# Performance work log

Measured on AMD Instinct MI355X. Metric: run time of the kernel, lower is better.

## Reference

```python
import jax, jax.numpy as jnp
import numpy as np

B = 8            # scenes per batch
N_PER = 100_000  # voxels per scene
C_IN = 32
C_OUT = 64
GRID = 128       # voxel grid extent per axis
K = 8            # 2x2x2 kernel offsets
EPS = 1e-5


def _kernel_maps():
    """Build stride-2 sparse-conv kernel maps (MinkowskiEngine semantics).

    Each input voxel at coord c maps to output voxel floor(c/2) with kernel
    offset c - 2*floor(c/2) in {0,1}^3.
    """
    rng = np.random.default_rng(0)
    coords = rng.integers(0, GRID, size=(B * N_PER, 3)).astype(np.int64)
    batch = np.repeat(np.arange(B, dtype=np.int64), N_PER)
    out_c = coords // 2
    off = coords - 2 * out_c                      # {0,1}^3
    k_idx = off[:, 0] * 4 + off[:, 1] * 2 + off[:, 2]
    half = GRID // 2
    key = ((batch * half + out_c[:, 0]) * half + out_c[:, 1]) * half + out_c[:, 2]
    _, out_idx = np.unique(key, return_inverse=True)
    num_out = int(out_idx.max()) + 1
    return k_idx.astype(np.int32), out_idx.astype(np.int32), num_out


def setup_inputs() -> dict:
    k_idx_np, out_idx_np, num_out = _kernel_maps()
    key = jax.random.key(0)
    k1, k2, k3 = jax.random.split(key, 3)
    x = jax.random.normal(k1, (B * N_PER, C_IN), dtype=jnp.float32)
    W = jax.random.normal(k2, (K, C_IN, C_OUT), dtype=jnp.float32) * 0.05
    bias = jax.random.normal(k3, (C_OUT,), dtype=jnp.float32) * 0.01
    gamma = jnp.ones((C_OUT,), dtype=jnp.float32)
    beta = jnp.zeros((C_OUT,), dtype=jnp.float32)
    return {
        "x": x, "W": W, "bias": bias, "gamma": gamma, "beta": beta,
        "k_idx": jnp.asarray(k_idx_np), "out_idx": jnp.asarray(out_idx_np),
        "num_out": num_out,
    }


def reference(x, W, bias, gamma, beta, k_idx, out_idx, num_out):
    # Sparse conv (gather-GEMM-scatter). Each input voxel uses exactly one of
    # the 8 kernel weights (stride==kernel_size==2), so y[i] = x[i] @ W[k_idx[i]].
    y = jnp.zeros((x.shape[0], W.shape[2]), dtype=x.dtype)
    for j in range(K):  # small fixed loop over kernel offsets
        y = y + jnp.where((k_idx == j)[:, None], x @ W[j], 0.0)
    out = jax.ops.segment_sum(y, out_idx, num_segments=num_out) + bias
    # BatchNorm (training-mode batch stats over output voxels) + ReLU
    mean = out.mean(axis=0)
    var = out.var(axis=0)
    out = (out - mean) * jax.lax.rsqrt(var + EPS) * gamma + beta
    return jax.nn.relu(out)
```

## Files before the change

kernel.cpp:

```cpp
#include <hip/hip_runtime.h>

#define EPS_BN 1e-5f

typedef __attribute__((ext_vector_type(8))) short short8;
typedef __attribute__((ext_vector_type(4))) float floatx4;

__device__ __forceinline__ short f2bf(float f) {
    unsigned u = __float_as_uint(f);
    u += 0x7FFF + ((u >> 16) & 1);
    return (short)(u >> 16);
}


__global__ void pack_W(const float* __restrict__ W, short* __restrict__ packed)
{
    const int s = blockIdx.x * 256 + threadIdx.x;
    const int j = s >> 8, t = (s >> 6) & 3, l = s & 63;
    const int k0 = (l >> 4) * 8, c = (l & 15) + 16 * t;
    short8 v;
#pragma unroll
    for (int i = 0; i < 8; ++i)
        v[i] = f2bf(W[(j * 32 + k0 + i) * 64 + c]);
    ((short8*)packed)[s] = v;
}

__global__ void scatter_slots(const int* __restrict__ out_idx,
                              const int* __restrict__ k_idx,
                              int* __restrict__ slot, int* __restrict__ next,
                              unsigned* __restrict__ chainmask, int n)
{
    int i = blockIdx.x * 256 + threadIdx.x;
    if (i < n) {
        const int o = out_idx[i];
        const int k = k_idx[i];
        int old = atomicExch(&slot[(size_t)o * 8 + k], i);
        next[i] = old;
        if (old >= 0) atomicOr(&chainmask[o], 1u << k);
    }
}

__global__ __launch_bounds__(512, 8) void gather_mfma(
    const float* __restrict__ x, const short* __restrict__ packedW,
    const int* __restrict__ slot, const int* __restrict__ next_arr,
    const unsigned* __restrict__ chainmask,
    float* __restrict__ out, float* __restrict__ partials,
    int num_out, int nb)
{
    __shared__ short sW[16384];
    __shared__ float s_stat[128];

    const int tid = threadIdx.x;
    if (tid < 128) s_stat[tid] = 0.f;
    for (int i = tid; i < 2048; i += 512)
        ((short8*)sW)[i] = ((const short8*)packedW)[i];
    __syncthreads();

    const int wave = tid >> 6, lane = tid & 63;
    const int quad = lane >> 4, row = lane & 15;
    const int obase = blockIdx.x * 128 + wave * 16;
    const int o = obase + row;
    const bool valid_o = (o < num_out);

    int4 sl0 = make_int4(-1, -1, -1, -1), sl1 = sl0;
    unsigned cm = 0u;
    if (valid_o) {
        const int4* sp = (const int4*)(slot + (size_t)o * 8);
        sl0 = sp[0]; sl1 = sp[1];
        cm = chainmask[o];
    }

    floatx4 acc[4] = {{0,0,0,0},{0,0,0,0},{0,0,0,0},{0,0,0,0}};
    const short8* bw = (const short8*)sW;

#pragma unroll
    for (int j = 0; j < 8; ++j) {
        const int v = (j < 4) ? ((j == 0) ? sl0.x : (j == 1) ? sl0.y : (j == 2) ? sl0.z : sl0.w)
                              : ((j == 4) ? sl1.x : (j == 5) ? sl1.y : (j == 6) ? sl1.z : sl1.w);
        if (!__any(v >= 0)) continue;
        float4 xa = make_float4(0.f, 0.f, 0.f, 0.f), xb = xa;
        if (v >= 0) {
            const float4* xp = (const float4*)(x + (size_t)v * 32) + quad * 2;
            xa = xp[0]; xb = xp[1];
        }
        if (__any((cm >> j) & 1u)) {
            int w = (v >= 0 && ((cm >> j) & 1u)) ? next_arr[v] : -1;
            while (__any(w >= 0)) {
                if (w >= 0) {
                    const float4* xp2 = (const float4*)(x + (size_t)w * 32) + quad * 2;
                    float4 ya = xp2[0], yb = xp2[1];
                    xa.x += ya.x; xa.y += ya.y; xa.z += ya.z; xa.w += ya.w;
                    xb.x += yb.x; xb.y += yb.y; xb.z += yb.z; xb.w += yb.w;
                    w = next_arr[w];
                }
            }
        }
        short8 afrag;
        afrag[0] = f2bf(xa.x); afrag[1] = f2bf(xa.y);
        afrag[2] = f2bf(xa.z); afrag[3] = f2bf(xa.w);
        afrag[4] = f2bf(xb.x); afrag[5] = f2bf(xb.y);
        afrag[6] = f2bf(xb.z); afrag[7] = f2bf(xb.w);

        const int jb = j * 256;
#pragma unroll
        for (int t = 0; t < 4; ++t) {
            const short8 bfrag = bw[jb + t * 64 + lane];
            acc[t] = __builtin_amdgcn_mfma_f32_16x16x32_bf16(afrag, bfrag, acc[t], 0, 0, 0);
        }
    }

#pragma unroll
    for (int t = 0; t < 4; ++t) {
        const int c = (lane & 15) + 16 * t;
        float sum = 0.f, sq = 0.f;
#pragma unroll
        for (int r = 0; r < 4; ++r) {
            const int oc = obase + quad * 4 + r;
            const float val = acc[t][r];
            if (oc < num_out) {
                out[(size_t)oc * 64 + c] = val;
                sum += val; sq += val * val;
            }
        }
        sum += __shfl_xor(sum, 16, 64); sum += __shfl_xor(sum, 32, 64);
        sq  += __shfl_xor(sq, 16, 64);  sq  += __shfl_xor(sq, 32, 64);
        if (quad == 0) {
            atomicAdd(&s_stat[c], sum);
            atomicAdd(&s_stat[64 + c], sq);
        }
    }
    __syncthreads();
    if (tid < 128) partials[(size_t)tid * nb + blockIdx.x] = s_stat[tid];
}

__global__ __launch_bounds__(256) void reduce_finalize(
    const float* __restrict__ partials, const float* __restrict__ gamma,
    const float* __restrict__ beta, float* __restrict__ ws_ab,
    int nb, float inv_n)
{
    __shared__ float r1[256], r2[256];
    const int c = blockIdx.x, t = threadIdx.x;
    float s1 = 0.f, s2 = 0.f;
    for (int i = t; i < nb; i += 256) {
        s1 += partials[(size_t)c * nb + i];
        s2 += partials[(size_t)(c + 64) * nb + i];
    }
    r1[t] = s1; r2[t] = s2;
    __syncthreads();
    for (int d = 128; d > 0; d >>= 1) {
        if (t < d) { r1[t] += r1[t + d]; r2[t] += r2[t + d]; }
        __syncthreads();
    }
    if (t == 0) {
        const float mean = r1[0] * inv_n;
        const float var = r2[0] * inv_n - mean * mean;
        const float a = gamma[c] * rsqrtf(var + EPS_BN);
        ws_ab[c] = a;
        ws_ab[64 + c] = beta[c] - mean * a;
    }
}

__global__ __launch_bounds__(256) void apply_kernel(
    float* __restrict__ out, const float* __restrict__ ws_ab, int n4)
{
    const int tid = blockIdx.x * 256 + threadIdx.x;
    const int stride = gridDim.x * 256;
    const int cg = tid & 15;
    const float4 a = ((const float4*)ws_ab)[cg];
    const float4 b = ((const float4*)(ws_ab + 64))[cg];
    float4* o4 = (float4*)out;
    for (int i = tid; i < n4; i += stride) {
        float4 v = o4[i];
        v.x = fmaxf(fmaf(v.x, a.x, b.x), 0.f);
        v.y = fmaxf(fmaf(v.y, a.y, b.y), 0.f);
        v.z = fmaxf(fmaf(v.z, a.z, b.z), 0.f);
        v.w = fmaxf(fmaf(v.w, a.w, b.w), 0.f);
        o4[i] = v;
    }
}

extern "C" void kernel_launch(void* const* d_in, const int* in_sizes, int n_in,
                              void* d_out, int out_size, void* d_ws, size_t ws_size,
                              hipStream_t stream)
{
    const float* x     = (const float*)d_in[0];
    const float* W     = (const float*)d_in[1];
    const float* gamma = (const float*)d_in[3];
    const float* beta  = (const float*)d_in[4];
    const int* k_idx   = (const int*)d_in[5];
    const int* out_idx = (const int*)d_in[6];

    const int n_vox   = in_sizes[5];
    const int num_out = out_size / 64;
    const int nb      = (num_out + 127) / 128;
    float* out = (float*)d_out;

    char* p = (char*)d_ws;
    float* ws_ab    = (float*)(p + 512);
    short* packedW  = (short*)(p + 1024);
    float* partials = (float*)(p + 1024 + 32768);
    char*  p2       = p + 1024 + 32768 + (size_t)128 * nb * 4;
    int*   slot     = (int*)p2;
    int*   next     = slot + (size_t)num_out * 8;
    unsigned* chainmask = (unsigned*)(next + n_vox);

    hipMemsetAsync(slot, 0xFF, (size_t)num_out * 8 * sizeof(int), stream);
    hipMemsetAsync(chainmask, 0, (size_t)num_out * sizeof(unsigned), stream);

    pack_W        <<<8, 256, 0, stream>>>(W, packedW);
    scatter_slots <<<(n_vox + 255) / 256, 256, 0, stream>>>(out_idx, k_idx, slot, next, chainmask, n_vox);
    gather_mfma   <<<nb, 512, 0, stream>>>(x, packedW, slot, next, chainmask, out, partials, num_out, nb);
    reduce_finalize<<<64, 256, 0, stream>>>(partials, gamma, beta, ws_ab, nb, 1.0f / (float)num_out);
    apply_kernel  <<<1024, 256, 0, stream>>>(out, ws_ab, out_size / 4);
}
```

Baseline: 408.4 us.

## Make gather kernel persistent over tiles and make x loads unconditional

The gather-MFMA kernel now launches at most 1024 blocks that loop over 128-row output tiles. Each block amortises its shared-memory weight load and accumulates BN statistics in registers across tiles, so fewer partials reach the reduce kernel. The x row loads are now issued unconditionally with a clamped index instead of behind a wave-vote skip, and the chain walk is marked unlikely. The apply kernel's grid is raised to 4096 blocks. The risks are lower occupancy or worse latency hiding from fewer resident blocks, and extra loads of row 0 for empty slots.

```diff
diff --git a/kernel.cpp b/kernel.cpp
--- a/kernel.cpp
+++ b/kernel.cpp
@@ -44,7 +44,7 @@
     const int* __restrict__ slot, const int* __restrict__ next_arr,
     const unsigned* __restrict__ chainmask,
     float* __restrict__ out, float* __restrict__ partials,
-    int num_out, int nb)
+    int num_out, int ntiles)
 {
     __shared__ short sW[16384];
     __shared__ float s_stat[128];
@@ -57,79 +57,92 @@
 
     const int wave = tid >> 6, lane = tid & 63;
     const int quad = lane >> 4, row = lane & 15;
-    const int obase = blockIdx.x * 128 + wave * 16;
-    const int o = obase + row;
-    const bool valid_o = (o < num_out);
-
-    int4 sl0 = make_int4(-1, -1, -1, -1), sl1 = sl0;
-    unsigned cm = 0u;
-    if (valid_o) {
-        const int4* sp = (const int4*)(slot + (size_t)o * 8);
-        sl0 = sp[0]; sl1 = sp[1];
-        cm = chainmask[o];
-    }
-
-    floatx4 acc[4] = {{0,0,0,0},{0,0,0,0},{0,0,0,0},{0,0,0,0}};
     const short8* bw = (const short8*)sW;
-
-#pragma unroll
-    for (int j = 0; j < 8; ++j) {
-        const int v = (j < 4) ? ((j == 0) ? sl0.x : (j == 1) ? sl0.y : (j == 2) ? sl0.z : sl0.w)
-                              : ((j == 4) ? sl1.x : (j == 5) ? sl1.y : (j == 6) ? sl1.z : sl1.w);
-        if (!__any(v >= 0)) continue;
-        float4 xa = make_float4(0.f, 0.f, 0.f, 0.f), xb = xa;
-        if (v >= 0) {
-            const float4* xp = (const float4*)(x + (size_t)v * 32) + quad * 2;
-            xa = xp[0]; xb = xp[1];
-        }
-        if (__any((cm >> j) & 1u)) {
-            int w = (v >= 0 && ((cm >> j) & 1u)) ? next_arr[v] : -1;
-            while (__any(w >= 0)) {
-                if (w >= 0) {
-                    const float4* xp2 = (const float4*)(x + (size_t)w * 32) + quad * 2;
-                    float4 ya = xp2[0], yb = xp2[1];
-                    xa.x += ya.x; xa.y += ya.y; xa.z += ya.z; xa.w += ya.w;
-                    xb.x += yb.x; xb.y += yb.y; xb.z += yb.z; xb.w += yb.w;
-                    w = next_arr[w];
+    const float4* xq = (const float4*)x + quad * 2;
+
+    float statS[4] = {0.f, 0.f, 0.f, 0.f};
+    float statQ[4] = {0.f, 0.f, 0.f, 0.f};
+
+    for (int tile = blockIdx.x; tile < ntiles; tile += gridDim.x) {
+        const int obase = tile * 128 + wave * 16;
+        const int o = obase + row;
+        const bool valid_o = (o < num_out);
+
+        int4 sl0 = make_int4(-1, -1, -1, -1), sl1 = sl0;
+        unsigned cm = 0u;
+        if (valid_o) {
+            const int4* sp = (const int4*)(slot + (size_t)o * 8);
+            sl0 = sp[0]; sl1 = sp[1];
+            cm = chainmask[o];
+        }
+        const int sl[8] = {sl0.x, sl0.y, sl0.z, sl0.w, sl1.x, sl1.y, sl1.z, sl1.w};
+
+        floatx4 acc[4] = {{0,0,0,0},{0,0,0,0},{0,0,0,0},{0,0,0,0}};
+
+#pragma unroll
+        for (int j = 0; j < 8; ++j) {
+            const int v = sl[j];
+            const float4* xp = xq + (size_t)(v < 0 ? 0 : v) * 8;
+            float4 xa = xp[0], xb = xp[1];
+            if (v < 0) {
+                xa = make_float4(0.f, 0.f, 0.f, 0.f);
+                xb = make_float4(0.f, 0.f, 0.f, 0.f);
+            }
+            if (__builtin_expect(__any((cm >> j) & 1u), 0)) {
+                int w = (v >= 0 && ((cm >> j) & 1u)) ? next_arr[v] : -1;
+                while (__any(w >= 0)) {
+                    if (w >= 0) {
+                        const float4* xp2 = xq + (size_t)w * 8;
+                        float4 ya = xp2[0], yb = xp2[1];
+                        xa.x += ya.x; xa.y += ya.y; xa.z += ya.z; xa.w += ya.w;
+                        xb.x += yb.x; xb.y += yb.y; xb.z += yb.z; xb.w += yb.w;
+                        w = next_arr[w];
+                    }
                 }
             }
-        }
-        short8 afrag;
-        afrag[0] = f2bf(xa.x); afrag[1] = f2bf(xa.y);
-        afrag[2] = f2bf(xa.z); afrag[3] = f2bf(xa.w);
-        afrag[4] = f2bf(xb.x); afrag[5] = f2bf(xb.y);
-        afrag[6] = f2bf(xb.z); afrag[7] = f2bf(xb.w);
-
-        const int jb = j * 256;
+            short8 afrag;
+            afrag[0] = f2bf(xa.x); afrag[1] = f2bf(xa.y);
+            afrag[2] = f2bf(xa.z); afrag[3] = f2bf(xa.w);
+            afrag[4] = f2bf(xb.x); afrag[5] = f2bf(xb.y);
+            afrag[6] = f2bf(xb.z); afrag[7] = f2bf(xb.w);
+
+            const int jb = j * 256;
+#pragma unroll
+            for (int t = 0; t < 4; ++t) {
+                const short8 bfrag = bw[jb + t * 64 + lane];
+                acc[t] = __builtin_amdgcn_mfma_f32_16x16x32_bf16(afrag, bfrag, acc[t], 0, 0, 0);
+            }
+        }
+
 #pragma unroll
         for (int t = 0; t < 4; ++t) {
-            const short8 bfrag = bw[jb + t * 64 + lane];
-            acc[t] = __builtin_amdgcn_mfma_f32_16x16x32_bf16(afrag, bfrag, acc[t], 0, 0, 0);
+            const int c = (lane & 15) + 16 * t;
+#pragma unroll
+            for (int r = 0; r < 4; ++r) {
+                const int oc = obase + quad * 4 + r;
+                const float val = acc[t][r];
+                if (oc < num_out) {
+                    out[(size_t)oc * 64 + c] = val;
+                    statS[t] += val;
+                    statQ[t] += val * val;
+                }
+            }
         }
     }
 
 #pragma unroll
     for (int t = 0; t < 4; ++t) {
-        const int c = (lane & 15) + 16 * t;
-        float sum = 0.f, sq = 0.f;
-#pragma unroll
-        for (int r = 0; r < 4; ++r) {
-            const int oc = obase + quad * 4 + r;
-            const float val = acc[t][r];
-            if (oc < num_out) {
-                out[(size_t)oc * 64 + c] = val;
-                sum += val; sq += val * val;
-            }
-        }
+        float sum = statS[t], sq = statQ[t];
         sum += __shfl_xor(sum, 16, 64); sum += __shfl_xor(sum, 32, 64);
         sq  += __shfl_xor(sq, 16, 64);  sq  += __shfl_xor(sq, 32, 64);
         if (quad == 0) {
+            const int c = (lane & 15) + 16 * t;
             atomicAdd(&s_stat[c], sum);
             atomicAdd(&s_stat[64 + c], sq);
         }
     }
     __syncthreads();
-    if (tid < 128) partials[(size_t)tid * nb + blockIdx.x] = s_stat[tid];
+    if (tid < 128) partials[(size_t)tid * gridDim.x + blockIdx.x] = s_stat[tid];
 }
 
 __global__ __launch_bounds__(256) void reduce_finalize(
@@ -191,14 +204,15 @@
 
     const int n_vox   = in_sizes[5];
     const int num_out = out_size / 64;
-    const int nb      = (num_out + 127) / 128;
+    const int ntiles  = (num_out + 127) / 128;
+    const int nbg     = (ntiles < 1024) ? ntiles : 1024;
     float* out = (float*)d_out;
 
     char* p = (char*)d_ws;
     float* ws_ab    = (float*)(p + 512);
     short* packedW  = (short*)(p + 1024);
     float* partials = (float*)(p + 1024 + 32768);
-    char*  p2       = p + 1024 + 32768 + (size_t)128 * nb * 4;
+    char*  p2       = p + 1024 + 32768 + (size_t)128 * 1024 * 4;
     int*   slot     = (int*)p2;
     int*   next     = slot + (size_t)num_out * 8;
     unsigned* chainmask = (unsigned*)(next + n_vox);
@@ -208,7 +222,7 @@
 
     pack_W        <<<8, 256, 0, stream>>>(W, packedW);
     scatter_slots <<<(n_vox + 255) / 256, 256, 0, stream>>>(out_idx, k_idx, slot, next, chainmask, n_vox);
-    gather_mfma   <<<nb, 512, 0, stream>>>(x, packedW, slot, next, chainmask, out, partials, num_out, nb);
-    reduce_finalize<<<64, 256, 0, stream>>>(partials, gamma, beta, ws_ab, nb, 1.0f / (float)num_out);
-    apply_kernel  <<<1024, 256, 0, stream>>>(out, ws_ab, out_size / 4);
-}
+    gather_mfma   <<<nbg, 512, 0, stream>>>(x, packedW, slot, next, chainmask, out, partials, num_out, ntiles);
+    reduce_finalize<<<64, 256, 0, stream>>>(partials, gamma, beta, ws_ab, nbg, 1.0f / (float)num_out);
+    apply_kernel  <<<4096, 256, 0, stream>>>(out, ws_ab, out_size / 4);
+}
```

Measured after the change: 734.0 us. 1.8x slower.

## Fuse weight packing into scatter kernel and merge memsets via inverted chain mask

Applied to the files above, without the earlier changes.

Packing the weights now happens in the first blocks of the scatter kernel, and the chain mask is stored inverted (initialised to all ones, cleared with atomicAnd). The mask is laid out right after the slot table, so a single 0xFF memset initialises both and one launch and one memset are removed. In the gather kernel the slot and mask loads are issued before the shared-memory weight copy and barrier so their latency overlaps, and the chain-walk branch is marked unlikely. The apply kernel uses nontemporal stores and a larger grid. Together these trade a little extra work in the scatter blocks for fewer launches and better latency hiding.

```diff
diff --git a/kernel.cpp b/kernel.cpp
--- a/kernel.cpp
+++ b/kernel.cpp
@@ -12,37 +12,37 @@
 }
 
 
-__global__ void pack_W(const float* __restrict__ W, short* __restrict__ packed)
-{
-    const int s = blockIdx.x * 256 + threadIdx.x;
-    const int j = s >> 8, t = (s >> 6) & 3, l = s & 63;
-    const int k0 = (l >> 4) * 8, c = (l & 15) + 16 * t;
-    short8 v;
-#pragma unroll
-    for (int i = 0; i < 8; ++i)
-        v[i] = f2bf(W[(j * 32 + k0 + i) * 64 + c]);
-    ((short8*)packed)[s] = v;
-}
-
-__global__ void scatter_slots(const int* __restrict__ out_idx,
-                              const int* __restrict__ k_idx,
-                              int* __restrict__ slot, int* __restrict__ next,
-                              unsigned* __restrict__ chainmask, int n)
-{
-    int i = blockIdx.x * 256 + threadIdx.x;
+__global__ void scatter_pack(const int* __restrict__ out_idx,
+                             const int* __restrict__ k_idx,
+                             const float* __restrict__ W,
+                             int* __restrict__ slot, int* __restrict__ next,
+                             unsigned* __restrict__ cm_inv,
+                             short* __restrict__ packed, int n)
+{
+    const int i = blockIdx.x * 256 + threadIdx.x;
+    if (blockIdx.x < 8) {
+        const int s = i;
+        const int j = s >> 8, t = (s >> 6) & 3, l = s & 63;
+        const int k0 = (l >> 4) * 8, c = (l & 15) + 16 * t;
+        short8 v;
+#pragma unroll
+        for (int q = 0; q < 8; ++q)
+            v[q] = f2bf(W[(j * 32 + k0 + q) * 64 + c]);
+        ((short8*)packed)[s] = v;
+    }
     if (i < n) {
         const int o = out_idx[i];
         const int k = k_idx[i];
         int old = atomicExch(&slot[(size_t)o * 8 + k], i);
         next[i] = old;
-        if (old >= 0) atomicOr(&chainmask[o], 1u << k);
+        if (old >= 0) atomicAnd(&cm_inv[o], ~(1u << k));
     }
 }
 
 __global__ __launch_bounds__(512, 8) void gather_mfma(
     const float* __restrict__ x, const short* __restrict__ packedW,
     const int* __restrict__ slot, const int* __restrict__ next_arr,
-    const unsigned* __restrict__ chainmask,
+    const unsigned* __restrict__ cm_inv,
     float* __restrict__ out, float* __restrict__ partials,
     int num_out, int nb)
 {
@@ -50,11 +50,6 @@
     __shared__ float s_stat[128];
 
     const int tid = threadIdx.x;
-    if (tid < 128) s_stat[tid] = 0.f;
-    for (int i = tid; i < 2048; i += 512)
-        ((short8*)sW)[i] = ((const short8*)packedW)[i];
-    __syncthreads();
-
     const int wave = tid >> 6, lane = tid & 63;
     const int quad = lane >> 4, row = lane & 15;
     const int obase = blockIdx.x * 128 + wave * 16;
@@ -62,12 +57,19 @@
     const bool valid_o = (o < num_out);
 
     int4 sl0 = make_int4(-1, -1, -1, -1), sl1 = sl0;
-    unsigned cm = 0u;
+    unsigned cmraw = 0xFFFFFFFFu;
     if (valid_o) {
         const int4* sp = (const int4*)(slot + (size_t)o * 8);
         sl0 = sp[0]; sl1 = sp[1];
-        cm = chainmask[o];
-    }
+        cmraw = cm_inv[o];
+    }
+
+    if (tid < 128) s_stat[tid] = 0.f;
+    for (int i = tid; i < 2048; i += 512)
+        ((short8*)sW)[i] = ((const short8*)packedW)[i];
+    __syncthreads();
+
+    const unsigned cm = ~cmraw;
 
     floatx4 acc[4] = {{0,0,0,0},{0,0,0,0},{0,0,0,0},{0,0,0,0}};
     const short8* bw = (const short8*)sW;
@@ -82,7 +84,7 @@
             const float4* xp = (const float4*)(x + (size_t)v * 32) + quad * 2;
             xa = xp[0]; xb = xp[1];
         }
-        if (__any((cm >> j) & 1u)) {
+        if (__builtin_expect(__any((cm >> j) & 1u), 0)) {
             int w = (v >= 0 && ((cm >> j) & 1u)) ? next_arr[v] : -1;
             while (__any(w >= 0)) {
                 if (w >= 0) {
@@ -165,16 +167,16 @@
     const int tid = blockIdx.x * 256 + threadIdx.x;
     const int stride = gridDim.x * 256;
     const int cg = tid & 15;
-    const float4 a = ((const float4*)ws_ab)[cg];
-    const float4 b = ((const float4*)(ws_ab + 64))[cg];
-    float4* o4 = (float4*)out;
+    const floatx4 a = ((const floatx4*)ws_ab)[cg];
+    const floatx4 b = ((const floatx4*)(ws_ab + 64))[cg];
+    floatx4* o4 = (floatx4*)out;
     for (int i = tid; i < n4; i += stride) {
-        float4 v = o4[i];
+        floatx4 v = o4[i];
         v.x = fmaxf(fmaf(v.x, a.x, b.x), 0.f);
         v.y = fmaxf(fmaf(v.y, a.y, b.y), 0.f);
         v.z = fmaxf(fmaf(v.z, a.z, b.z), 0.f);
         v.w = fmaxf(fmaf(v.w, a.w, b.w), 0.f);
-        o4[i] = v;
+        __builtin_nontemporal_store(v, o4 + i);
     }
 }
 
@@ -200,15 +202,14 @@
     float* partials = (float*)(p + 1024 + 32768);
     char*  p2       = p + 1024 + 32768 + (size_t)128 * nb * 4;
     int*   slot     = (int*)p2;
-    int*   next     = slot + (size_t)num_out * 8;
-    unsigned* chainmask = (unsigned*)(next + n_vox);
-
-    hipMemsetAsync(slot, 0xFF, (size_t)num_out * 8 * sizeof(int), stream);
-    hipMemsetAsync(chainmask, 0, (size_t)num_out * sizeof(unsigned), stream);
-
-    pack_W        <<<8, 256, 0, stream>>>(W, packedW);
-    scatter_slots <<<(n_vox + 255) / 256, 256, 0, stream>>>(out_idx, k_idx, slot, next, chainmask, n_vox);
-    gather_mfma   <<<nb, 512, 0, stream>>>(x, packedW, slot, next, chainmask, out, partials, num_out, nb);
+    unsigned* cm_inv = (unsigned*)(slot + (size_t)num_out * 8);
+    int*   next     = (int*)(cm_inv + num_out);
+
+    (void)hipMemsetAsync(slot, 0xFF, (size_t)num_out * 9 * sizeof(int), stream);
+
+    const int nsb = (n_vox + 255) / 256;
+    scatter_pack  <<<nsb, 256, 0, stream>>>(out_idx, k_idx, W, slot, next, cm_inv, packedW, n_vox);
+    gather_mfma   <<<nb, 512, 0, stream>>>(x, packedW, slot, next, cm_inv, out, partials, num_out, nb);
     reduce_finalize<<<64, 256, 0, stream>>>(partials, gamma, beta, ws_ab, nb, 1.0f / (float)num_out);
-    apply_kernel  <<<1024, 256, 0, stream>>>(out, ws_ab, out_size / 4);
-}
+    apply_kernel  <<<4096, 256, 0, stream>>>(out, ws_ab, out_size / 4);
+}
```

After: 404.6 us. About the same (-0.9%).
